# Kernel optimization log

Measured on AMD Instinct MI355X. Metric: run time of the kernel, lower is better.

The kernel has to match this reference:

```python
import jax, jax.numpy as jnp
import numpy as np

B, N, D, BS = 2, 4096, 2048, 256  # batch, seq, d_model, chunk size


def rms_norm(x):
    eps = jnp.asarray(jnp.finfo(x.dtype).eps, x.dtype)
    return x * jax.lax.rsqrt(jnp.mean(x * x, axis=-1, keepdims=True) + eps)


def la_kernel(q, k, v, bs):
    # chunked linear attention: intra-chunk masked QK^T + cross-chunk KV recurrence
    b, n, d = q.shape
    T = n // bs
    qc = q.reshape(b, T, bs, d).transpose(1, 0, 2, 3)  # [T,B,bs,d]
    kc = k.reshape(b, T, bs, d).transpose(1, 0, 2, 3)
    vc = v.reshape(b, T, bs, d).transpose(1, 0, 2, 3)
    mask = jnp.tril(jnp.ones((bs, bs), q.dtype))

    def step(kv, qkv):
        qt, kt, vt = qkv  # each [B,bs,d]
        s = jnp.einsum('bid,bjd->bij', qt, kt) * mask        # masked intra-chunk scores
        ot = jnp.einsum('bij,bjd->bid', s, vt) + jnp.einsum('bid,bde->bie', qt, kv)
        kv = kv + jnp.einsum('bjd,bje->bde', kt, vt)          # state update AFTER output
        return kv, ot

    kv0 = jnp.zeros((b, d, d), q.dtype)
    _, o = jax.lax.scan(step, kv0, (qc, kc, vc))              # o: [T,B,bs,d]
    return o.transpose(1, 0, 2, 3).reshape(b, n, d)


def setup_inputs() -> dict:
    key = jax.random.key(0)
    ks = jax.random.split(key, 6)
    scale = 0.02
    x = jax.random.normal(ks[0], (B, N, D), jnp.float32)
    Wq = jax.random.normal(ks[1], (D, D), jnp.float32) * scale
    Wk = jax.random.normal(ks[2], (D, D), jnp.float32) * scale
    Wv = jax.random.normal(ks[3], (D, D), jnp.float32) * scale
    Wg = jax.random.normal(ks[4], (D, D), jnp.float32) * scale
    Wp = jax.random.normal(ks[5], (D, D), jnp.float32) * scale
    return {'x': x, 'Wq': Wq, 'Wk': Wk, 'Wv': Wv, 'Wg': Wg, 'Wp': Wp}


def reference(x, Wq, Wk, Wv, Wg, Wp):
    # weights stored torch-style (out,in): y = x @ W^T
    xn = rms_norm(x)
    q = jax.nn.silu(jnp.einsum('bnd,od->bno', xn, Wq))
    k = jax.nn.silu(jnp.einsum('bnd,od->bno', xn, Wk))
    v = jax.nn.silu(jnp.einsum('bnd,od->bno', xn, Wv))
    g = jax.nn.sigmoid(jnp.einsum('bnd,od->bno', xn, Wg))
    o = la_kernel(q, k, v, BS) * g
    return jnp.einsum('bnd,od->bno', o, Wp)
```

## Files before the change

### kernel.cpp

```cpp
#include <hip/hip_runtime.h>
#include <hip/hip_bf16.h>

typedef __bf16 bf16;
typedef __bf16 bf16x8 __attribute__((ext_vector_type(8)));
typedef float f32x4 __attribute__((ext_vector_type(4)));
typedef unsigned int u32;

#define D_    2048
#define NSEQ  4096
#define BATCH 2
#define CH    1024
#define TC    4
#define MROWS 8192

__device__ __forceinline__ void gload16(const bf16* g, bf16* l) {
  __builtin_amdgcn_global_load_lds(
      (const __attribute__((address_space(1))) u32*)g,
      (__attribute__((address_space(3))) u32*)l, 16, 0, 0);
}


struct SmemTiles {
  alignas(16) bf16 As[2][128 * 32];
  alignas(16) bf16 Bs[2][128 * 32];
};

__device__ __forceinline__ void stage128(SmemTiles& sm, int bb, const bf16* A,
                                         int lda, const bf16* B, int ldb,
                                         int k0, int tid) {
#pragma unroll
  for (int it = 0; it < 2; ++it) {
    int c = it * 256 + tid;
    int r = c >> 2;
    int co = (c & 3) << 3;
    gload16(A + (size_t)r * lda + k0 + co, &sm.As[bb][c * 8]);
    gload16(B + (size_t)r * ldb + k0 + co, &sm.Bs[bb][c * 8]);
  }
}

__device__ __forceinline__ void gemm_core(SmemTiles& sm, const bf16* A, int lda,
                                          const bf16* B, int ldb, int K,
                                          f32x4 acc[4][4]) {
  const int tid = threadIdx.x;
  const int lane = tid & 63;
  const int wave = tid >> 6;
  const int wr = wave >> 1, wc = wave & 1;
  const int l15 = lane & 15, kl = lane >> 4;
  const int NT = K >> 5;
  if (NT <= 0) return;

  stage128(sm, 0, A, lda, B, ldb, 0, tid);
  __syncthreads();

  const int ao = (wr * 64 + l15) * 32 + kl * 8;
  const int bo = (wc * 64 + l15) * 32 + kl * 8;

  for (int t = 0; t < NT; ++t) {
    if (t + 1 < NT)
      stage128(sm, (t + 1) & 1, A, lda, B, ldb, (t + 1) * 32, tid);
    const bf16* Ab = sm.As[t & 1];
    const bf16* Bb = sm.Bs[t & 1];
    bf16x8 a[4], b[4];
#pragma unroll
    for (int m = 0; m < 4; ++m) a[m] = *(const bf16x8*)(Ab + ao + m * 16 * 32);
#pragma unroll
    for (int n = 0; n < 4; ++n) b[n] = *(const bf16x8*)(Bb + bo + n * 16 * 32);
    __builtin_amdgcn_s_setprio(1);
#pragma unroll
    for (int m = 0; m < 4; ++m)
#pragma unroll
      for (int n = 0; n < 4; ++n)
        acc[m][n] = __builtin_amdgcn_mfma_f32_16x16x32_bf16(a[m], b[n], acc[m][n], 0, 0, 0);
    __builtin_amdgcn_s_setprio(0);
    if (t + 1 < NT) __syncthreads();
  }
}

#define EPILOGUE_VARS                              \
  const int lane = threadIdx.x & 63;               \
  const int wave = threadIdx.x >> 6;               \
  const int wr = wave >> 1, wc = wave & 1;         \
  const int l15 = lane & 15, kl = lane >> 4;


struct SmemW {
  alignas(16) bf16 A[2][128 * 32];
  alignas(16) bf16 B[2][256 * 32];
};

__device__ __forceinline__ void stageW(SmemW& sm, int bb, const bf16* A,
                                       int lda, const bf16* B, int ldb,
                                       int k0, int wave, int lane) {
  const int r16 = lane & 15, c8 = lane >> 4;
  gload16(A + (size_t)(wave * 16 + r16) * lda + k0 + c8 * 8,
          &sm.A[bb][wave * 512 + lane * 8]);
#pragma unroll
  for (int j = 0; j < 2; ++j) {
    int nb = 2 * wave + j;
    gload16(B + (size_t)(nb * 16 + r16) * ldb + k0 + c8 * 8,
            &sm.B[bb][nb * 512 + lane * 8]);
  }
}

__device__ __forceinline__ void gemmW_core(SmemW& sm, const bf16* A, int lda,
                                           const bf16* B, int ldb, int K,
                                           f32x4 acc[4][4]) {
  const int tid = threadIdx.x;
  const int wave = tid >> 6, lane = tid & 63;
  const int wr = wave >> 2, wc = wave & 3;
  const int NT = K >> 5;
  if (NT <= 0) return;

  stageW(sm, 0, A, lda, B, ldb, 0, wave, lane);
  if (NT > 1) {
    stageW(sm, 1, A, lda, B, ldb, 32, wave, lane);
    asm volatile("s_waitcnt vmcnt(3)" ::: "memory");
  } else {
    asm volatile("s_waitcnt vmcnt(0)" ::: "memory");
  }
  __builtin_amdgcn_s_barrier();

  const int aoff = wr * 2048 + lane * 8;
  const int boff = wc * 2048 + lane * 8;

  for (int t = 0; t < NT; ++t) {
    const bf16* Ab = sm.A[t & 1];
    const bf16* Bb = sm.B[t & 1];
    bf16x8 av[4], bv[4];
#pragma unroll
    for (int m = 0; m < 4; ++m) av[m] = *(const bf16x8*)&Ab[aoff + m * 512];
#pragma unroll
    for (int n = 0; n < 4; ++n) bv[n] = *(const bf16x8*)&Bb[boff + n * 512];
    asm volatile("s_waitcnt lgkmcnt(0)" ::: "memory");
    __builtin_amdgcn_s_barrier();
    if (t + 2 < NT)
      stageW(sm, t & 1, A, lda, B, ldb, (t + 2) * 32, wave, lane);
    __builtin_amdgcn_s_setprio(1);
#pragma unroll
    for (int m = 0; m < 4; ++m)
#pragma unroll
      for (int n = 0; n < 4; ++n)
        acc[m][n] = __builtin_amdgcn_mfma_f32_16x16x32_bf16(av[m], bv[n],
                                                            acc[m][n], 0, 0, 0);
    __builtin_amdgcn_s_setprio(0);
    if (t + 1 < NT) {
      if (t + 2 < NT)
        asm volatile("s_waitcnt vmcnt(3)" ::: "memory");
      else
        asm volatile("s_waitcnt vmcnt(0)" ::: "memory");
      __builtin_amdgcn_s_barrier();
    }
  }
}

#define EPILOGUEW_VARS                             \
  const int lane = threadIdx.x & 63;               \
  const int wave = threadIdx.x >> 6;               \
  const int wr = wave >> 2, wc = wave & 3;         \
  const int l15 = lane & 15, kl = lane >> 4;


__global__ __launch_bounds__(256) void k_f2b(const float* __restrict__ in,
                                             bf16* __restrict__ out) {
  int i = (blockIdx.x * 256 + threadIdx.x) * 8;
  float4 a = *(const float4*)(in + i);
  float4 b = *(const float4*)(in + i + 4);
  bf16x8 o;
  o[0] = (bf16)a.x; o[1] = (bf16)a.y; o[2] = (bf16)a.z; o[3] = (bf16)a.w;
  o[4] = (bf16)b.x; o[5] = (bf16)b.y; o[6] = (bf16)b.z; o[7] = (bf16)b.w;
  *(bf16x8*)(out + i) = o;
}

__global__ __launch_bounds__(256) void k_f2b2(const float* __restrict__ in0,
                                              const float* __restrict__ in1,
                                              bf16* __restrict__ out) {
  int i = (blockIdx.x * 256 + threadIdx.x) * 8;
  const float* src = (i < D_ * D_) ? in0 : in1;
  int off = (i < D_ * D_) ? i : i - D_ * D_;
  float4 a = *(const float4*)(src + off);
  float4 b = *(const float4*)(src + off + 4);
  bf16x8 o;
  o[0] = (bf16)a.x; o[1] = (bf16)a.y; o[2] = (bf16)a.z; o[3] = (bf16)a.w;
  o[4] = (bf16)b.x; o[5] = (bf16)b.y; o[6] = (bf16)b.z; o[7] = (bf16)b.w;
  *(bf16x8*)(out + i) = o;
}

__global__ __launch_bounds__(256) void k_rms(const float* __restrict__ x,
                                             bf16* __restrict__ xn) {
  const int row = blockIdx.x;
  const int tid = threadIdx.x;
  const float* xr = x + (size_t)row * D_;
  float4 a = *(const float4*)(xr + tid * 8);
  float4 b = *(const float4*)(xr + tid * 8 + 4);
  float ss = a.x * a.x + a.y * a.y + a.z * a.z + a.w * a.w +
             b.x * b.x + b.y * b.y + b.z * b.z + b.w * b.w;
#pragma unroll
  for (int o = 32; o > 0; o >>= 1) ss += __shfl_xor(ss, o, 64);
  __shared__ float red[4];
  if ((tid & 63) == 0) red[tid >> 6] = ss;
  __syncthreads();
  float tot = red[0] + red[1] + red[2] + red[3];
  float sc = rsqrtf(tot * (1.f / D_) + 1.1920928955078125e-07f);
  bf16x8 o;
  o[0] = (bf16)(a.x * sc); o[1] = (bf16)(a.y * sc);
  o[2] = (bf16)(a.z * sc); o[3] = (bf16)(a.w * sc);
  o[4] = (bf16)(b.x * sc); o[5] = (bf16)(b.y * sc);
  o[6] = (bf16)(b.z * sc); o[7] = (bf16)(b.w * sc);
  *(bf16x8*)(xn + (size_t)row * D_ + tid * 8) = o;
}


template <int ACT, int SMODE>
__global__ __launch_bounds__(512, 4) void k_proj2(const bf16* __restrict__ xn,
                                                  const bf16* __restrict__ W,
                                                  bf16* __restrict__ Cn,
                                                  bf16* __restrict__ Ct) {
  __shared__ SmemW sm;
  const int row0 = blockIdx.y * 128, col0 = blockIdx.x * 256;
  f32x4 acc[4][4] = {};
  gemmW_core(sm, xn + (size_t)row0 * D_, D_, W + (size_t)col0 * D_, D_, D_, acc);
  EPILOGUEW_VARS
#pragma unroll
  for (int m = 0; m < 4; ++m)
#pragma unroll
    for (int n = 0; n < 4; ++n)
#pragma unroll
      for (int j = 0; j < 4; ++j) {
        int r = row0 + wr * 64 + m * 16 + kl * 4 + j;
        int c = col0 + wc * 64 + n * 16 + l15;
        float v = acc[m][n][j];
        if (ACT == 1) v = v / (1.f + __expf(-v));
        if (ACT == 2) v = 1.f / (1.f + __expf(-v));
        bf16 ob = (bf16)v;
        if (SMODE & 1) Cn[(size_t)r * D_ + c] = ob;
        if (SMODE & 2)
          Ct[((size_t)(r >> 12) * D_ + c) * NSEQ + (r & (NSEQ - 1))] = ob;
      }
}

__global__ __launch_bounds__(512, 4) void k_final2(const bf16* __restrict__ og,
                                                   const bf16* __restrict__ Wp,
                                                   float* __restrict__ out) {
  __shared__ SmemW sm;
  const int row0 = blockIdx.y * 128, col0 = blockIdx.x * 256;
  f32x4 acc[4][4] = {};
  gemmW_core(sm, og + (size_t)row0 * D_, D_, Wp + (size_t)col0 * D_, D_, D_, acc);
  EPILOGUEW_VARS
#pragma unroll
  for (int m = 0; m < 4; ++m)
#pragma unroll
    for (int n = 0; n < 4; ++n)
#pragma unroll
      for (int j = 0; j < 4; ++j) {
        int r = row0 + wr * 64 + m * 16 + kl * 4 + j;
        int c = col0 + wc * 64 + n * 16 + l15;
        out[(size_t)r * D_ + c] = acc[m][n][j];
      }
}


__global__ __launch_bounds__(256) void k_scores(const bf16* __restrict__ q,
                                                const bf16* __restrict__ k,
                                                bf16* __restrict__ s) {
  const int z = blockIdx.z, b = z >> 2, t = z & 3;
  const int row0 = blockIdx.y * 128, col0 = blockIdx.x * 128;
  if (col0 > row0) return;
  __shared__ SmemTiles sm;
  f32x4 acc[4][4] = {};
  gemm_core(sm, q + (size_t)(b * NSEQ + t * CH + row0) * D_, D_,
                k + (size_t)(b * NSEQ + t * CH + col0) * D_, D_, D_, acc);
  EPILOGUE_VARS
  bf16* sp = s + (size_t)z * CH * CH;
#pragma unroll
  for (int m = 0; m < 4; ++m)
#pragma unroll
    for (int n = 0; n < 4; ++n)
#pragma unroll
      for (int j = 0; j < 4; ++j) {
        int i = row0 + wr * 64 + m * 16 + kl * 4 + j;
        int jc = col0 + wc * 64 + n * 16 + l15;
        float v = (i >= jc) ? acc[m][n][j] : 0.f;
        sp[(size_t)i * CH + jc] = (bf16)v;
      }
}

__global__ __launch_bounds__(256) void k_ointra(const bf16* __restrict__ s,
                                                const bf16* __restrict__ vT,
                                                bf16* __restrict__ og) {
  __shared__ SmemTiles sm;
  const int z = blockIdx.z, b = z >> 2, t = z & 3;
  const int row0 = blockIdx.y * 128, col0 = blockIdx.x * 128;
  const int K = row0 + 128;
  f32x4 acc[4][4] = {};
  gemm_core(sm, s + (size_t)z * CH * CH + (size_t)row0 * CH, CH,
                vT + (size_t)b * D_ * NSEQ + (size_t)col0 * NSEQ + t * CH, NSEQ,
                K, acc);
  EPILOGUE_VARS
#pragma unroll
  for (int m = 0; m < 4; ++m)
#pragma unroll
    for (int n = 0; n < 4; ++n)
#pragma unroll
      for (int j = 0; j < 4; ++j) {
        int i = row0 + wr * 64 + m * 16 + kl * 4 + j;
        int c = col0 + wc * 64 + n * 16 + l15;
        og[(size_t)(b * NSEQ + t * CH + i) * D_ + c] = (bf16)acc[m][n][j];
      }
}

__global__ __launch_bounds__(256) void k_ointer(const bf16* __restrict__ q,
                                                const bf16* __restrict__ kvb,
                                                const bf16* __restrict__ g,
                                                bf16* __restrict__ og, int t,
                                                int Kin) {
  __shared__ SmemTiles sm;
  const int b = blockIdx.z;
  const int row0 = blockIdx.y * 128, col0 = blockIdx.x * 128;
  f32x4 acc[4][4] = {};
  gemm_core(sm, q + (size_t)(b * NSEQ + t * CH + row0) * D_, D_,
                kvb + (size_t)b * D_ * D_ + (size_t)col0 * D_, D_, Kin, acc);
  EPILOGUE_VARS
#pragma unroll
  for (int m = 0; m < 4; ++m)
#pragma unroll
    for (int n = 0; n < 4; ++n)
#pragma unroll
      for (int j = 0; j < 4; ++j) {
        int i = row0 + wr * 64 + m * 16 + kl * 4 + j;
        int c = col0 + wc * 64 + n * 16 + l15;
        size_t idx = (size_t)(b * NSEQ + t * CH + i) * D_ + c;
        float v = ((float)og[idx] + acc[m][n][j]) * (float)g[idx];
        og[idx] = (bf16)v;
      }
}

__global__ __launch_bounds__(256) void k_update(const bf16* __restrict__ vT,
                                                const bf16* __restrict__ kT,
                                                bf16* __restrict__ kvb, int t) {
  __shared__ SmemTiles sm;
  const int b = blockIdx.z;
  const int row0 = blockIdx.y * 128, col0 = blockIdx.x * 128;
  f32x4 acc[4][4] = {};
  gemm_core(sm, vT + (size_t)b * D_ * NSEQ + (size_t)row0 * NSEQ + t * CH, NSEQ,
                kT + (size_t)b * D_ * NSEQ + (size_t)col0 * NSEQ + t * CH, NSEQ,
                CH, acc);
  EPILOGUE_VARS
#pragma unroll
  for (int m = 0; m < 4; ++m)
#pragma unroll
    for (int n = 0; n < 4; ++n)
#pragma unroll
      for (int j = 0; j < 4; ++j) {
        int e = row0 + wr * 64 + m * 16 + kl * 4 + j;
        int d = col0 + wc * 64 + n * 16 + l15;
        size_t idx = (size_t)b * D_ * D_ + (size_t)e * D_ + d;
        float v = acc[m][n][j];
        if (t > 0) v += (float)kvb[idx];
        kvb[idx] = (bf16)v;
      }
}


extern "C" void kernel_launch(void* const* d_in, const int* in_sizes, int n_in,
                              void* d_out, int out_size, void* d_ws, size_t ws_size,
                              hipStream_t stream) {
  (void)in_sizes; (void)n_in; (void)out_size; (void)ws_size;
  const float* x  = (const float*)d_in[0];
  const float* Wq = (const float*)d_in[1];
  const float* Wk = (const float*)d_in[2];
  const float* Wv = (const float*)d_in[3];
  const float* Wg = (const float*)d_in[4];
  const float* Wp = (const float*)d_in[5];
  float* out = (float*)d_out;

  char* p = (char*)d_ws;
  auto take = [&](size_t bytes) {
    char* r = p;
    p += (bytes + 255) & ~(size_t)255;
    return r;
  };
  const size_t MD2 = (size_t)MROWS * D_ * 2;

  bf16* xn  = (bf16*)take(MD2);
  bf16* kT  = (bf16*)take(MD2);
  bf16* vT  = (bf16*)take(MD2);
  bf16* k   = (bf16*)take((size_t)MROWS * D_ * 2);
  char* shared = take((size_t)BATCH * TC * CH * CH * 2);
  bf16* Wpair = (bf16*)shared;
  bf16* s    = (bf16*)shared;
  bf16* kvb  = (bf16*)shared;
  bf16* og = xn;

  bf16* q = (bf16*)d_out;
  bf16* g = (bf16*)d_out + (size_t)MROWS * D_;

  const size_t W1 = (size_t)D_ * D_;
  dim3 gpW(D_ / 256, MROWS / 128);

  k_rms<<<MROWS, 256, 0, stream>>>(x, xn);

  k_f2b2<<<2 * (D_ * D_) / 2048, 256, 0, stream>>>(Wq, Wk, Wpair);
  k_proj2<1, 1><<<gpW, 512, 0, stream>>>(xn, Wpair, q, (bf16*)nullptr);
  k_proj2<1, 3><<<gpW, 512, 0, stream>>>(xn, Wpair + W1, k, kT);
  k_f2b2<<<2 * (D_ * D_) / 2048, 256, 0, stream>>>(Wv, Wg, Wpair);
  k_proj2<1, 2><<<gpW, 512, 0, stream>>>(xn, Wpair, (bf16*)nullptr, vT);
  k_proj2<2, 1><<<gpW, 512, 0, stream>>>(xn, Wpair + W1, g, (bf16*)nullptr);

  k_scores<<<dim3(CH / 128, CH / 128, BATCH * TC), 256, 0, stream>>>(q, k, s);
  k_ointra<<<dim3(D_ / 128, CH / 128, BATCH * TC), 256, 0, stream>>>(s, vT, og);

  for (int t = 0; t < TC; ++t) {
    k_ointer<<<dim3(D_ / 128, CH / 128, BATCH), 256, 0, stream>>>(
        q, kvb, g, og, t, t ? D_ : 0);
    if (t < TC - 1)
      k_update<<<dim3(D_ / 128, D_ / 128, BATCH), 256, 0, stream>>>(vT, kT,
                                                                    kvb, t);
  }

  bf16* Wpb = (bf16*)shared;
  k_f2b<<<(D_ * D_) / 2048, 256, 0, stream>>>(Wp, Wpb);
  k_final2<<<gpW, 512, 0, stream>>>(og, Wpb, out);
}
```

Before: 872.4 us.

## Use 256x256 triple-buffered GEMM tiles for projections and skip empty first inter-chunk pass

The projection and output GEMMs move from 128x256 tiles with double buffering to 256x256 tiles with a three-stage LDS ring. Each wave now computes 128x64 and splits the k-step into two MFMA halves, with loads for later stages issued in between. This raises reuse per byte loaded and hides more latency, at the cost of more registers and LDS, so occupancy drops to 2 blocks per CU. Separately, the t=0 inter-chunk GEMM, which multiplied by a zero state, is removed; the gate is instead applied in the intra-chunk epilogue for chunk 0.

```diff
diff --git a/kernel.cpp b/kernel.cpp
--- a/kernel.cpp
+++ b/kernel.cpp
@@ -83,69 +83,90 @@
   const int l15 = lane & 15, kl = lane >> 4;
 
 
-struct SmemW {
-  alignas(16) bf16 A[2][128 * 32];
-  alignas(16) bf16 B[2][256 * 32];
+struct Smem3 {
+  alignas(16) bf16 A[3][256 * 32];
+  alignas(16) bf16 B[3][256 * 32];
 };
 
-__device__ __forceinline__ void stageW(SmemW& sm, int bb, const bf16* A,
-                                       int lda, const bf16* B, int ldb,
+__device__ __forceinline__ void stage3(bf16* buf, const bf16* G, int ldg,
                                        int k0, int wave, int lane) {
   const int r16 = lane & 15, c8 = lane >> 4;
-  gload16(A + (size_t)(wave * 16 + r16) * lda + k0 + c8 * 8,
-          &sm.A[bb][wave * 512 + lane * 8]);
 #pragma unroll
   for (int j = 0; j < 2; ++j) {
-    int nb = 2 * wave + j;
-    gload16(B + (size_t)(nb * 16 + r16) * ldb + k0 + c8 * 8,
-            &sm.B[bb][nb * 512 + lane * 8]);
-  }
-}
-
-__device__ __forceinline__ void gemmW_core(SmemW& sm, const bf16* A, int lda,
+    int s = 2 * wave + j;
+    gload16(G + (size_t)(s * 16 + r16) * ldg + k0 + c8 * 8,
+            buf + s * 512 + lane * 8);
+  }
+}
+
+__device__ __forceinline__ void gemm3_core(Smem3& sm, const bf16* A, int lda,
                                            const bf16* B, int ldb, int K,
-                                           f32x4 acc[4][4]) {
+                                           f32x4 acc[8][4]) {
   const int tid = threadIdx.x;
   const int wave = tid >> 6, lane = tid & 63;
   const int wr = wave >> 2, wc = wave & 3;
   const int NT = K >> 5;
   if (NT <= 0) return;
 
-  stageW(sm, 0, A, lda, B, ldb, 0, wave, lane);
+  stage3(sm.A[0], A, lda, 0, wave, lane);
+  stage3(sm.B[0], B, ldb, 0, wave, lane);
   if (NT > 1) {
-    stageW(sm, 1, A, lda, B, ldb, 32, wave, lane);
-    asm volatile("s_waitcnt vmcnt(3)" ::: "memory");
+    stage3(sm.A[1], A, lda, 32, wave, lane);
+    stage3(sm.B[1], B, ldb, 32, wave, lane);
+    asm volatile("s_waitcnt vmcnt(4)" ::: "memory");
   } else {
     asm volatile("s_waitcnt vmcnt(0)" ::: "memory");
   }
   __builtin_amdgcn_s_barrier();
 
-  const int aoff = wr * 2048 + lane * 8;
-  const int boff = wc * 2048 + lane * 8;
+  const int abase = wr * 8 * 512 + lane * 8;
+  const int bbase = wc * 4 * 512 + lane * 8;
 
   for (int t = 0; t < NT; ++t) {
-    const bf16* Ab = sm.A[t & 1];
-    const bf16* Bb = sm.B[t & 1];
+    const bf16* Ab = sm.A[t % 3];
+    const bf16* Bb = sm.B[t % 3];
+    const bool pf = (t + 2 < NT);
+    const int kn = (t + 2) * 32;
+    const int nb = (t + 2) % 3;
     bf16x8 av[4], bv[4];
-#pragma unroll
-    for (int m = 0; m < 4; ++m) av[m] = *(const bf16x8*)&Ab[aoff + m * 512];
-#pragma unroll
-    for (int n = 0; n < 4; ++n) bv[n] = *(const bf16x8*)&Bb[boff + n * 512];
+
+    if (pf) stage3(sm.A[nb], A, lda, kn, wave, lane);
+#pragma unroll
+    for (int nf = 0; nf < 4; ++nf) bv[nf] = *(const bf16x8*)&Bb[bbase + nf * 512];
+#pragma unroll
+    for (int mf = 0; mf < 4; ++mf) av[mf] = *(const bf16x8*)&Ab[abase + mf * 512];
+    __builtin_amdgcn_s_barrier();
     asm volatile("s_waitcnt lgkmcnt(0)" ::: "memory");
+    __builtin_amdgcn_sched_barrier(0);
+    __builtin_amdgcn_s_setprio(1);
+#pragma unroll
+    for (int mf = 0; mf < 4; ++mf)
+#pragma unroll
+      for (int nf = 0; nf < 4; ++nf)
+        acc[mf][nf] = __builtin_amdgcn_mfma_f32_16x16x32_bf16(av[mf], bv[nf],
+                                                              acc[mf][nf], 0, 0, 0);
+    __builtin_amdgcn_s_setprio(0);
     __builtin_amdgcn_s_barrier();
-    if (t + 2 < NT)
-      stageW(sm, t & 1, A, lda, B, ldb, (t + 2) * 32, wave, lane);
+
+    if (pf) stage3(sm.B[nb], B, ldb, kn, wave, lane);
+#pragma unroll
+    for (int mf = 0; mf < 4; ++mf)
+      av[mf] = *(const bf16x8*)&Ab[abase + (mf + 4) * 512];
+    __builtin_amdgcn_s_barrier();
+    asm volatile("s_waitcnt lgkmcnt(0)" ::: "memory");
+    __builtin_amdgcn_sched_barrier(0);
     __builtin_amdgcn_s_setprio(1);
 #pragma unroll
-    for (int m = 0; m < 4; ++m)
-#pragma unroll
-      for (int n = 0; n < 4; ++n)
-        acc[m][n] = __builtin_amdgcn_mfma_f32_16x16x32_bf16(av[m], bv[n],
-                                                            acc[m][n], 0, 0, 0);
+    for (int mf = 0; mf < 4; ++mf)
+#pragma unroll
+      for (int nf = 0; nf < 4; ++nf)
+        acc[mf + 4][nf] = __builtin_amdgcn_mfma_f32_16x16x32_bf16(av[mf], bv[nf],
+                                                                  acc[mf + 4][nf], 0, 0, 0);
     __builtin_amdgcn_s_setprio(0);
+
     if (t + 1 < NT) {
-      if (t + 2 < NT)
-        asm volatile("s_waitcnt vmcnt(3)" ::: "memory");
+      if (pf)
+        asm volatile("s_waitcnt vmcnt(4)" ::: "memory");
       else
         asm volatile("s_waitcnt vmcnt(0)" ::: "memory");
       __builtin_amdgcn_s_barrier();
@@ -153,7 +174,7 @@
   }
 }
 
-#define EPILOGUEW_VARS                             \
+#define EPILOGUE256_VARS                           \
   const int lane = threadIdx.x & 63;               \
   const int wave = threadIdx.x >> 6;               \
   const int wr = wave >> 2, wc = wave & 3;         \
@@ -211,24 +232,24 @@
 
 
 template <int ACT, int SMODE>
-__global__ __launch_bounds__(512, 4) void k_proj2(const bf16* __restrict__ xn,
+__global__ __launch_bounds__(512, 2) void k_proj2(const bf16* __restrict__ xn,
                                                   const bf16* __restrict__ W,
                                                   bf16* __restrict__ Cn,
                                                   bf16* __restrict__ Ct) {
-  __shared__ SmemW sm;
-  const int row0 = blockIdx.y * 128, col0 = blockIdx.x * 256;
-  f32x4 acc[4][4] = {};
-  gemmW_core(sm, xn + (size_t)row0 * D_, D_, W + (size_t)col0 * D_, D_, D_, acc);
-  EPILOGUEW_VARS
-#pragma unroll
-  for (int m = 0; m < 4; ++m)
-#pragma unroll
-    for (int n = 0; n < 4; ++n)
-#pragma unroll
-      for (int j = 0; j < 4; ++j) {
-        int r = row0 + wr * 64 + m * 16 + kl * 4 + j;
-        int c = col0 + wc * 64 + n * 16 + l15;
-        float v = acc[m][n][j];
+  __shared__ Smem3 sm;
+  const int row0 = blockIdx.y * 256, col0 = blockIdx.x * 256;
+  f32x4 acc[8][4] = {};
+  gemm3_core(sm, xn + (size_t)row0 * D_, D_, W + (size_t)col0 * D_, D_, D_, acc);
+  EPILOGUE256_VARS
+#pragma unroll
+  for (int mf = 0; mf < 8; ++mf)
+#pragma unroll
+    for (int nf = 0; nf < 4; ++nf)
+#pragma unroll
+      for (int j = 0; j < 4; ++j) {
+        int r = row0 + wr * 128 + mf * 16 + kl * 4 + j;
+        int c = col0 + wc * 64 + nf * 16 + l15;
+        float v = acc[mf][nf][j];
         if (ACT == 1) v = v / (1.f + __expf(-v));
         if (ACT == 2) v = 1.f / (1.f + __expf(-v));
         bf16 ob = (bf16)v;
@@ -238,23 +259,23 @@
       }
 }
 
-__global__ __launch_bounds__(512, 4) void k_final2(const bf16* __restrict__ og,
+__global__ __launch_bounds__(512, 2) void k_final2(const bf16* __restrict__ og,
                                                    const bf16* __restrict__ Wp,
                                                    float* __restrict__ out) {
-  __shared__ SmemW sm;
-  const int row0 = blockIdx.y * 128, col0 = blockIdx.x * 256;
-  f32x4 acc[4][4] = {};
-  gemmW_core(sm, og + (size_t)row0 * D_, D_, Wp + (size_t)col0 * D_, D_, D_, acc);
-  EPILOGUEW_VARS
-#pragma unroll
-  for (int m = 0; m < 4; ++m)
-#pragma unroll
-    for (int n = 0; n < 4; ++n)
-#pragma unroll
-      for (int j = 0; j < 4; ++j) {
-        int r = row0 + wr * 64 + m * 16 + kl * 4 + j;
-        int c = col0 + wc * 64 + n * 16 + l15;
-        out[(size_t)r * D_ + c] = acc[m][n][j];
+  __shared__ Smem3 sm;
+  const int row0 = blockIdx.y * 256, col0 = blockIdx.x * 256;
+  f32x4 acc[8][4] = {};
+  gemm3_core(sm, og + (size_t)row0 * D_, D_, Wp + (size_t)col0 * D_, D_, D_, acc);
+  EPILOGUE256_VARS
+#pragma unroll
+  for (int mf = 0; mf < 8; ++mf)
+#pragma unroll
+    for (int nf = 0; nf < 4; ++nf)
+#pragma unroll
+      for (int j = 0; j < 4; ++j) {
+        int r = row0 + wr * 128 + mf * 16 + kl * 4 + j;
+        int c = col0 + wc * 64 + nf * 16 + l15;
+        out[(size_t)r * D_ + c] = acc[mf][nf][j];
       }
 }
 
@@ -286,6 +307,7 @@
 
 __global__ __launch_bounds__(256) void k_ointra(const bf16* __restrict__ s,
                                                 const bf16* __restrict__ vT,
+                                                const bf16* __restrict__ g,
                                                 bf16* __restrict__ og) {
   __shared__ SmemTiles sm;
   const int z = blockIdx.z, b = z >> 2, t = z & 3;
@@ -296,6 +318,7 @@
                 vT + (size_t)b * D_ * NSEQ + (size_t)col0 * NSEQ + t * CH, NSEQ,
                 K, acc);
   EPILOGUE_VARS
+  const bool gate0 = (t == 0);
 #pragma unroll
   for (int m = 0; m < 4; ++m)
 #pragma unroll
@@ -304,21 +327,23 @@
       for (int j = 0; j < 4; ++j) {
         int i = row0 + wr * 64 + m * 16 + kl * 4 + j;
         int c = col0 + wc * 64 + n * 16 + l15;
-        og[(size_t)(b * NSEQ + t * CH + i) * D_ + c] = (bf16)acc[m][n][j];
+        size_t idx = (size_t)(b * NSEQ + t * CH + i) * D_ + c;
+        float v = acc[m][n][j];
+        if (gate0) v *= (float)g[idx];
+        og[idx] = (bf16)v;
       }
 }
 
 __global__ __launch_bounds__(256) void k_ointer(const bf16* __restrict__ q,
                                                 const bf16* __restrict__ kvb,
                                                 const bf16* __restrict__ g,
-                                                bf16* __restrict__ og, int t,
-                                                int Kin) {
+                                                bf16* __restrict__ og, int t) {
   __shared__ SmemTiles sm;
   const int b = blockIdx.z;
   const int row0 = blockIdx.y * 128, col0 = blockIdx.x * 128;
   f32x4 acc[4][4] = {};
   gemm_core(sm, q + (size_t)(b * NSEQ + t * CH + row0) * D_, D_,
-                kvb + (size_t)b * D_ * D_ + (size_t)col0 * D_, D_, Kin, acc);
+                kvb + (size_t)b * D_ * D_ + (size_t)col0 * D_, D_, D_, acc);
   EPILOGUE_VARS
 #pragma unroll
   for (int m = 0; m < 4; ++m)
@@ -395,29 +420,28 @@
   bf16* g = (bf16*)d_out + (size_t)MROWS * D_;
 
   const size_t W1 = (size_t)D_ * D_;
-  dim3 gpW(D_ / 256, MROWS / 128);
+  dim3 gp2(D_ / 256, MROWS / 256);
 
   k_rms<<<MROWS, 256, 0, stream>>>(x, xn);
 
   k_f2b2<<<2 * (D_ * D_) / 2048, 256, 0, stream>>>(Wq, Wk, Wpair);
-  k_proj2<1, 1><<<gpW, 512, 0, stream>>>(xn, Wpair, q, (bf16*)nullptr);
-  k_proj2<1, 3><<<gpW, 512, 0, stream>>>(xn, Wpair + W1, k, kT);
+  k_proj2<1, 1><<<gp2, 512, 0, stream>>>(xn, Wpair, q, (bf16*)nullptr);
+  k_proj2<1, 3><<<gp2, 512, 0, stream>>>(xn, Wpair + W1, k, kT);
   k_f2b2<<<2 * (D_ * D_) / 2048, 256, 0, stream>>>(Wv, Wg, Wpair);
-  k_proj2<1, 2><<<gpW, 512, 0, stream>>>(xn, Wpair, (bf16*)nullptr, vT);
-  k_proj2<2, 1><<<gpW, 512, 0, stream>>>(xn, Wpair + W1, g, (bf16*)nullptr);
+  k_proj2<1, 2><<<gp2, 512, 0, stream>>>(xn, Wpair, (bf16*)nullptr, vT);
+  k_proj2<2, 1><<<gp2, 512, 0, stream>>>(xn, Wpair + W1, g, (bf16*)nullptr);
 
   k_scores<<<dim3(CH / 128, CH / 128, BATCH * TC), 256, 0, stream>>>(q, k, s);
-  k_ointra<<<dim3(D_ / 128, CH / 128, BATCH * TC), 256, 0, stream>>>(s, vT, og);
-
-  for (int t = 0; t < TC; ++t) {
-    k_ointer<<<dim3(D_ / 128, CH / 128, BATCH), 256, 0, stream>>>(
-        q, kvb, g, og, t, t ? D_ : 0);
-    if (t < TC - 1)
-      k_update<<<dim3(D_ / 128, D_ / 128, BATCH), 256, 0, stream>>>(vT, kT,
-                                                                    kvb, t);
+  k_ointra<<<dim3(D_ / 128, CH / 128, BATCH * TC), 256, 0, stream>>>(s, vT, g, og);
+
+  for (int t = 1; t < TC; ++t) {
+    k_update<<<dim3(D_ / 128, D_ / 128, BATCH), 256, 0, stream>>>(vT, kT,
+                                                                  kvb, t - 1);
+    k_ointer<<<dim3(D_ / 128, CH / 128, BATCH), 256, 0, stream>>>(q, kvb, g,
+                                                                  og, t);
   }
 
   bf16* Wpb = (bf16*)shared;
   k_f2b<<<(D_ * D_) / 2048, 256, 0, stream>>>(Wp, Wpb);
-  k_final2<<<gpW, 512, 0, stream>>>(og, Wpb, out);
-}
+  k_final2<<<gp2, 512, 0, stream>>>(og, Wpb, out);
+}
```

Result: no change. 879.3 us (median of 2 runs) (+0.8%).
